# Kernel tuning notes

Hardware: AMD Instinct MI355X
Metric: run time of the kernel (lower is better)

The kernel has to match this reference:

```python
import jax, jax.numpy as jnp
import numpy as np

B, G, GS = 1024, 2000, 25   # batch, num gene groups, group size
H1, H2, C = 1024, 512, 10
EPS = 1e-5


def _xavier(key, shape, fan_in, fan_out):
    lim = np.sqrt(6.0 / (fan_in + fan_out))
    return jax.random.uniform(key, shape, jnp.float32, -lim, lim)


def setup_inputs() -> dict:
    key = jax.random.key(0)
    ks = jax.random.split(key, 8)
    x = jax.random.normal(ks[0], (B, G * GS), jnp.float32)
    # per-group Linear(GS, 1) weights stacked -> block-diagonal grouped GEMM
    gene_w = _xavier(ks[1], (G, GS), GS, 1)
    gene_b = jnp.zeros((G,), jnp.float32)
    W1 = _xavier(ks[2], (G, H1), G, H1)
    b1 = jnp.zeros((H1,), jnp.float32)
    W2 = _xavier(ks[3], (H1, H2), H1, H2)
    b2 = jnp.zeros((H2,), jnp.float32)
    Wout = _xavier(ks[4], (H2, C), H2, C)
    bout = jnp.zeros((C,), jnp.float32)
    Wres = _xavier(ks[5], (G, C), G, C)
    bres = jnp.zeros((C,), jnp.float32)
    gamma1 = jnp.ones((H1,), jnp.float32); beta1 = jnp.zeros((H1,), jnp.float32)
    gamma2 = jnp.ones((H2,), jnp.float32); beta2 = jnp.zeros((H2,), jnp.float32)
    return dict(x=x, gene_w=gene_w, gene_b=gene_b, W1=W1, b1=b1,
                gamma1=gamma1, beta1=beta1, W2=W2, b2=b2,
                gamma2=gamma2, beta2=beta2, Wout=Wout, bout=bout,
                Wres=Wres, bres=bres)


def _batch_norm(h, gamma, beta):
    # training-mode BatchNorm1d: biased batch statistics over axis 0
    mu = jnp.mean(h, axis=0)
    var = jnp.mean(jnp.square(h - mu), axis=0)
    return gamma * (h - mu) * jax.lax.rsqrt(var + EPS) + beta


def reference(x, gene_w, gene_b, W1, b1, gamma1, beta1, W2, b2,
              gamma2, beta2, Wout, bout, Wres, bres):
    # fused replacement for the per-group Linear(GS,1)+ReLU loop + cat
    xg = x.reshape(B, G, GS)
    g = jax.nn.relu(jnp.einsum('bgk,gk->bg', xg, gene_w) + gene_b)  # [B, G]
    h1 = jax.nn.relu(_batch_norm(g @ W1 + b1, gamma1, beta1))       # [B, H1]
    h2 = jax.nn.relu(_batch_norm(h1 @ W2 + b2, gamma2, beta2))      # [B, H2]
    x_main = h2 @ Wout + bout                                       # [B, C]
    x_res = g @ Wres + bres                                         # [B, C]
    return jax.nn.softmax(x_main + x_res, axis=1)
```

## Files before the change

### kernel.cpp

```cpp
#include <hip/hip_runtime.h>
#include <math.h>

#define NB   1024
#define NG   2000
#define NGS  25
#define KP   2048
#define NH1  1024
#define NH2  512
#define NC   10
#define EPSV 1e-5f
#define GPB  200

typedef __attribute__((ext_vector_type(8))) __bf16 bf16x8;
typedef __attribute__((ext_vector_type(4))) float f32x4;
typedef __attribute__((ext_vector_type(8))) unsigned short u16x8;
typedef __attribute__((ext_vector_type(4))) unsigned short u16x4;

__device__ __forceinline__ unsigned short f2bf(float f) {
  union { float f; unsigned u; } v; v.f = f;
  return (unsigned short)((v.u + 0x7fffu + ((v.u >> 16) & 1u)) >> 16);
}
__device__ __forceinline__ float bf2f(unsigned short b) {
  union { unsigned u; float f; } v; v.u = ((unsigned)b) << 16;
  return v.f;
}

__global__ __launch_bounds__(256) void gene_kernel(
    const float* __restrict__ x, const float* __restrict__ gw,
    const float* __restrict__ gb, unsigned short* __restrict__ g_bf) {
  __shared__ float xs[GPB * NGS];
  int b = blockIdx.x;
  int blk = blockIdx.y;
  const float4* src = (const float4*)(x + (size_t)b * (NG * NGS) + blk * (GPB * NGS));
  float4* dst = (float4*)xs;
  for (int i = threadIdx.x; i < (GPB * NGS) / 4; i += 256) dst[i] = src[i];
  __syncthreads();
  int j = threadIdx.x;
  if (j < GPB) {
    int gi = blk * GPB + j;
    const float* wp = gw + gi * NGS;
    const float* xp = xs + j * NGS;
    float acc = 0.f;
#pragma unroll
    for (int k = 0; k < NGS; ++k) acc = fmaf(xp[k], wp[k], acc);
    acc += gb[gi];
    g_bf[(size_t)b * KP + gi] = f2bf(fmaxf(acc, 0.f));
  } else if (blk == (NG / GPB - 1) && j < GPB + (KP - NG)) {
    g_bf[(size_t)b * KP + NG + (j - GPB)] = 0;
  }
}

__global__ __launch_bounds__(256) void convT_dual(
    const float* __restrict__ W1, unsigned short* __restrict__ W1bT,
    const float* __restrict__ W2, unsigned short* __restrict__ W2bT) {
  const float* src; unsigned short* dst; int K, N, Kpad;
  if (blockIdx.z == 0) { src = W1; dst = W1bT; K = NG; N = NH1; Kpad = KP; }
  else {
    src = W2; dst = W2bT; K = NH1; N = NH2; Kpad = NH1;
    if (blockIdx.x >= NH1 / 64 || blockIdx.y >= NH2 / 64) return;
  }
  __shared__ unsigned short ts[64][72];
  int k0 = blockIdx.x * 64, n0 = blockIdx.y * 64;
  int t = threadIdx.x;
  int c4 = (t & 15) * 4;
  int r  = t >> 4;
  for (int rr = r; rr < 64; rr += 16) {
    int k = k0 + rr;
    float4 v = make_float4(0.f, 0.f, 0.f, 0.f);
    if (k < K) v = *(const float4*)&src[(size_t)k * N + n0 + c4];
    ts[rr][c4 + 0] = f2bf(v.x); ts[rr][c4 + 1] = f2bf(v.y);
    ts[rr][c4 + 2] = f2bf(v.z); ts[rr][c4 + 3] = f2bf(v.w);
  }
  __syncthreads();
  int rr8 = (t & 7) * 8;
  int cc  = t >> 3;
  for (int c = cc; c < 64; c += 32) {
    u16x8 val;
#pragma unroll
    for (int i = 0; i < 8; ++i) val[i] = ts[rr8 + i][c];
    *(u16x8*)&dst[(size_t)(n0 + c) * Kpad + k0 + rr8] = val;
  }
}

__global__ __launch_bounds__(256) void gemm1_kernel(
    const unsigned short* __restrict__ A,
    const unsigned short* __restrict__ Bt,
    float* __restrict__ C, float* __restrict__ sum, float* __restrict__ sq,
    int M, int N, int Kp) {
  __shared__ unsigned short As[64][72];
  __shared__ unsigned short Bs[64][72];
  int t = threadIdx.x;
  int m0 = blockIdx.y * 64, n0 = blockIdx.x * 64;
  int wave = t >> 6, lane = t & 63;
  int wm = (wave >> 1) * 32, wn = (wave & 1) * 32;
  int fm = lane & 15, fk = (lane >> 4) * 8;
  int srow = t >> 3, skc = (t & 7) * 8;

  f32x4 acc[2][2];
#pragma unroll
  for (int i = 0; i < 2; ++i)
#pragma unroll
    for (int j = 0; j < 2; ++j) acc[i][j] = (f32x4){0.f, 0.f, 0.f, 0.f};

  const unsigned short* Ap = A + (size_t)(m0 + srow) * Kp + skc;
  const unsigned short* Bp = Bt + (size_t)(n0 + srow) * Kp + skc;
  size_t rstep = 32 * (size_t)Kp;

  u16x8 pa0 = *(const u16x8*)(Ap);
  u16x8 pa1 = *(const u16x8*)(Ap + rstep);
  u16x8 pb0 = *(const u16x8*)(Bp);
  u16x8 pb1 = *(const u16x8*)(Bp + rstep);

  for (int k0 = 0; k0 < Kp; k0 += 64) {
    *(u16x8*)&As[srow][skc]      = pa0;
    *(u16x8*)&As[srow + 32][skc] = pa1;
    *(u16x8*)&Bs[srow][skc]      = pb0;
    *(u16x8*)&Bs[srow + 32][skc] = pb1;
    __syncthreads();
    if (k0 + 64 < Kp) {
      pa0 = *(const u16x8*)(Ap + k0 + 64);
      pa1 = *(const u16x8*)(Ap + k0 + 64 + rstep);
      pb0 = *(const u16x8*)(Bp + k0 + 64);
      pb1 = *(const u16x8*)(Bp + k0 + 64 + rstep);
    }
#pragma unroll
    for (int s = 0; s < 2; ++s) {
      bf16x8 af[2], bfr[2];
      af[0]  = *(const bf16x8*)&As[wm + fm][s * 32 + fk];
      af[1]  = *(const bf16x8*)&As[wm + 16 + fm][s * 32 + fk];
      bfr[0] = *(const bf16x8*)&Bs[wn + fm][s * 32 + fk];
      bfr[1] = *(const bf16x8*)&Bs[wn + 16 + fm][s * 32 + fk];
#pragma unroll
      for (int i = 0; i < 2; ++i)
#pragma unroll
        for (int j = 0; j < 2; ++j)
          acc[i][j] = __builtin_amdgcn_mfma_f32_16x16x32_bf16(
              af[i], bfr[j], acc[i][j], 0, 0, 0);
    }
    __syncthreads();
  }

  int crow = (lane >> 4) * 4, ccol = lane & 15;
#pragma unroll
  for (int j = 0; j < 2; ++j) {
    float s = 0.f, ss = 0.f;
#pragma unroll
    for (int i = 0; i < 2; ++i)
#pragma unroll
      for (int r = 0; r < 4; ++r) {
        float v = acc[i][j][r];
        int m = m0 + wm + i * 16 + crow + r;
        int n = n0 + wn + j * 16 + ccol;
        C[(size_t)m * N + n] = v;
        s += v;
        ss = fmaf(v, v, ss);
      }
    s  += __shfl_down(s, 32, 64);  s  += __shfl_down(s, 16, 64);
    ss += __shfl_down(ss, 32, 64); ss += __shfl_down(ss, 16, 64);
    if (lane < 16) {
      atomicAdd(&sum[n0 + wn + j * 16 + lane], s);
      atomicAdd(&sq[n0 + wn + j * 16 + lane], ss);
    }
  }
}

__global__ __launch_bounds__(256) void gemm2_kernel(
    const float* __restrict__ A,
    const unsigned short* __restrict__ Bt,
    float* __restrict__ C, const float* __restrict__ sum1,
    const float* __restrict__ sq1, const float* __restrict__ gam1,
    const float* __restrict__ bet1, float* __restrict__ sum2,
    float* __restrict__ sq2, int M, int N, int Kp) {
  __shared__ unsigned short As[64][72];
  __shared__ unsigned short Bs[64][72];
  int t = threadIdx.x;
  int m0 = blockIdx.y * 64, n0 = blockIdx.x * 64;
  int wave = t >> 6, lane = t & 63;
  int wm = (wave >> 1) * 32, wn = (wave & 1) * 32;
  int fm = lane & 15, fk = (lane >> 4) * 8;
  int srow = t >> 3, skc = (t & 7) * 8;

  f32x4 acc[2][2];
#pragma unroll
  for (int i = 0; i < 2; ++i)
#pragma unroll
    for (int j = 0; j < 2; ++j) acc[i][j] = (f32x4){0.f, 0.f, 0.f, 0.f};

  const float* Ap = A + (size_t)(m0 + srow) * Kp + skc;
  const unsigned short* Bp = Bt + (size_t)(n0 + srow) * Kp + skc;
  size_t rstepA = 32 * (size_t)Kp;
  size_t rstepB = 32 * (size_t)Kp;

  f32x4 pa[4];
  pa[0] = *(const f32x4*)(Ap);
  pa[1] = *(const f32x4*)(Ap + 4);
  pa[2] = *(const f32x4*)(Ap + rstepA);
  pa[3] = *(const f32x4*)(Ap + rstepA + 4);
  u16x8 pb0 = *(const u16x8*)(Bp);
  u16x8 pb1 = *(const u16x8*)(Bp + rstepB);

  for (int k0 = 0; k0 < Kp; k0 += 64) {
    float sc[8], sh[8];
#pragma unroll
    for (int i = 0; i < 8; ++i) {
      int k = k0 + skc + i;
      float mu  = sum1[k] * (1.f / NB);
      float var = sq1[k] * (1.f / NB) - mu * mu;
      float rs  = rsqrtf(var + EPSV);
      sc[i] = gam1[k] * rs;
      sh[i] = fmaf(-mu, sc[i], bet1[k]);
    }
    u16x8 a0, a1;
#pragma unroll
    for (int i = 0; i < 4; ++i) {
      a0[i]     = f2bf(fmaxf(fmaf(pa[0][i], sc[i],     sh[i]),     0.f));
      a0[i + 4] = f2bf(fmaxf(fmaf(pa[1][i], sc[i + 4], sh[i + 4]), 0.f));
      a1[i]     = f2bf(fmaxf(fmaf(pa[2][i], sc[i],     sh[i]),     0.f));
      a1[i + 4] = f2bf(fmaxf(fmaf(pa[3][i], sc[i + 4], sh[i + 4]), 0.f));
    }
    *(u16x8*)&As[srow][skc]      = a0;
    *(u16x8*)&As[srow + 32][skc] = a1;
    *(u16x8*)&Bs[srow][skc]      = pb0;
    *(u16x8*)&Bs[srow + 32][skc] = pb1;
    __syncthreads();
    if (k0 + 64 < Kp) {
      pa[0] = *(const f32x4*)(Ap + k0 + 64);
      pa[1] = *(const f32x4*)(Ap + k0 + 64 + 4);
      pa[2] = *(const f32x4*)(Ap + k0 + 64 + rstepA);
      pa[3] = *(const f32x4*)(Ap + k0 + 64 + rstepA + 4);
      pb0 = *(const u16x8*)(Bp + k0 + 64);
      pb1 = *(const u16x8*)(Bp + k0 + 64 + rstepB);
    }
#pragma unroll
    for (int s = 0; s < 2; ++s) {
      bf16x8 af[2], bfr[2];
      af[0]  = *(const bf16x8*)&As[wm + fm][s * 32 + fk];
      af[1]  = *(const bf16x8*)&As[wm + 16 + fm][s * 32 + fk];
      bfr[0] = *(const bf16x8*)&Bs[wn + fm][s * 32 + fk];
      bfr[1] = *(const bf16x8*)&Bs[wn + 16 + fm][s * 32 + fk];
#pragma unroll
      for (int i = 0; i < 2; ++i)
#pragma unroll
        for (int j = 0; j < 2; ++j)
          acc[i][j] = __builtin_amdgcn_mfma_f32_16x16x32_bf16(
              af[i], bfr[j], acc[i][j], 0, 0, 0);
    }
    __syncthreads();
  }

  int crow = (lane >> 4) * 4, ccol = lane & 15;
#pragma unroll
  for (int j = 0; j < 2; ++j) {
    float s = 0.f, ss = 0.f;
#pragma unroll
    for (int i = 0; i < 2; ++i)
#pragma unroll
      for (int r = 0; r < 4; ++r) {
        float v = acc[i][j][r];
        int m = m0 + wm + i * 16 + crow + r;
        int n = n0 + wn + j * 16 + ccol;
        C[(size_t)m * N + n] = v;
        s += v;
        ss = fmaf(v, v, ss);
      }
    s  += __shfl_down(s, 32, 64);  s  += __shfl_down(s, 16, 64);
    ss += __shfl_down(ss, 32, 64); ss += __shfl_down(ss, 16, 64);
    if (lane < 16) {
      atomicAdd(&sum2[n0 + wn + j * 16 + lane], s);
      atomicAdd(&sq2[n0 + wn + j * 16 + lane], ss);
    }
  }
}

__global__ __launch_bounds__(256) void final_kernel(
    const float* __restrict__ t2, const float* __restrict__ sum2,
    const float* __restrict__ sq2, const float* __restrict__ gam2,
    const float* __restrict__ bet2, const unsigned short* __restrict__ g_bf,
    const float* __restrict__ Wout, const float* __restrict__ bout,
    const float* __restrict__ Wres, const float* __restrict__ bres,
    float* __restrict__ out) {
  int b = blockIdx.x;
  int t = threadIdx.x;
  float acc[NC] = {};

  if (t < NH2 / 4) {
    float4 tv = *(const float4*)&t2[(size_t)b * NH2 + t * 4];
    float raw[4] = {tv.x, tv.y, tv.z, tv.w};
    float hr[4];
#pragma unroll
    for (int i = 0; i < 4; ++i) {
      int c = t * 4 + i;
      float mu  = sum2[c] * (1.f / NB);
      float var = sq2[c] * (1.f / NB) - mu * mu;
      float rs  = rsqrtf(var + EPSV);
      float scv = gam2[c] * rs;
      hr[i] = fmaxf(fmaf(raw[i], scv, fmaf(-mu, scv, bet2[c])), 0.f);
    }
    const float4* wp = (const float4*)&Wout[t * 4 * NC];
    float w[40];
#pragma unroll
    for (int q = 0; q < 10; ++q) {
      float4 wv = wp[q];
      w[q * 4] = wv.x; w[q * 4 + 1] = wv.y; w[q * 4 + 2] = wv.z; w[q * 4 + 3] = wv.w;
    }
#pragma unroll
    for (int r = 0; r < 4; ++r)
#pragma unroll
      for (int c = 0; c < NC; ++c) acc[c] = fmaf(hr[r], w[r * NC + c], acc[c]);
  }

  for (int u = t; u < NG / 4; u += 256) {
    u16x4 gv = *(const u16x4*)&g_bf[(size_t)b * KP + u * 4];
    float gr[4] = {bf2f(gv[0]), bf2f(gv[1]), bf2f(gv[2]), bf2f(gv[3])};
    const float4* wp = (const float4*)&Wres[u * 4 * NC];
    float w[40];
#pragma unroll
    for (int q = 0; q < 10; ++q) {
      float4 wv = wp[q];
      w[q * 4] = wv.x; w[q * 4 + 1] = wv.y; w[q * 4 + 2] = wv.z; w[q * 4 + 3] = wv.w;
    }
#pragma unroll
    for (int r = 0; r < 4; ++r)
#pragma unroll
      for (int c = 0; c < NC; ++c) acc[c] = fmaf(gr[r], w[r * NC + c], acc[c]);
  }

  __shared__ float red[4][NC];
  __shared__ float logits[NC];
  int lane = t & 63, wave = t >> 6;
#pragma unroll
  for (int c = 0; c < NC; ++c) {
    float v = acc[c];
    for (int off = 32; off > 0; off >>= 1) v += __shfl_down(v, off, 64);
    if (lane == 0) red[wave][c] = v;
  }
  __syncthreads();
  if (t < NC)
    logits[t] = red[0][t] + red[1][t] + red[2][t] + red[3][t] + bout[t] + bres[t];
  __syncthreads();
  if (t == 0) {
    float mx = logits[0];
#pragma unroll
    for (int c = 1; c < NC; ++c) mx = fmaxf(mx, logits[c]);
    float e[NC], s = 0.f;
#pragma unroll
    for (int c = 0; c < NC; ++c) { e[c] = expf(logits[c] - mx); s += e[c]; }
    float inv = 1.f / s;
#pragma unroll
    for (int c = 0; c < NC; ++c) out[(size_t)b * NC + c] = e[c] * inv;
  }
}

extern "C" void kernel_launch(void* const* d_in, const int* in_sizes, int n_in,
                              void* d_out, int out_size, void* d_ws, size_t ws_size,
                              hipStream_t stream) {
  const float* x      = (const float*)d_in[0];
  const float* gw     = (const float*)d_in[1];
  const float* gb     = (const float*)d_in[2];
  const float* W1     = (const float*)d_in[3];
  const float* gamma1 = (const float*)d_in[5];
  const float* beta1  = (const float*)d_in[6];
  const float* W2     = (const float*)d_in[7];
  const float* gamma2 = (const float*)d_in[9];
  const float* beta2  = (const float*)d_in[10];
  const float* Wout   = (const float*)d_in[11];
  const float* bout   = (const float*)d_in[12];
  const float* Wres   = (const float*)d_in[13];
  const float* bres   = (const float*)d_in[14];
  float* out = (float*)d_out;

  char* p = (char*)d_ws;
  unsigned short* g_bf = (unsigned short*)p; p += (size_t)NB * KP * 2;
  unsigned short* W1bT = (unsigned short*)p; p += (size_t)NH1 * KP * 2;
  unsigned short* W2bT = (unsigned short*)p; p += (size_t)NH2 * NH1 * 2;
  float* t1 = (float*)p; p += (size_t)NB * NH1 * 4;
  float* t2 = (float*)p; p += (size_t)NB * NH2 * 4;
  float* stats = (float*)p;
  float* sum1 = stats, *sq1 = stats + 1024, *sum2 = stats + 2048, *sq2 = stats + 2560;

  hipMemsetAsync(stats, 0, 3072 * sizeof(float), stream);

  convT_dual<<<dim3(KP / 64, NH1 / 64, 2), 256, 0, stream>>>(W1, W1bT, W2, W2bT);

  gene_kernel<<<dim3(NB, NG / GPB), 256, 0, stream>>>(x, gw, gb, g_bf);

  gemm1_kernel<<<dim3(NH1 / 64, NB / 64), 256, 0, stream>>>(
      g_bf, W1bT, t1, sum1, sq1, NB, NH1, KP);

  gemm2_kernel<<<dim3(NH2 / 64, NB / 64), 256, 0, stream>>>(
      t1, W2bT, t2, sum1, sq1, gamma1, beta1, sum2, sq2, NB, NH2, NH1);

  final_kernel<<<NB, 256, 0, stream>>>(t2, sum2, sq2, gamma2, beta2, g_bf,
                                       Wout, bout, Wres, bres, out);
}
```

Measured before the change: 372.5 us.

## Merge prep kernels into one launch and shrink GEMM tiles for more blocks

Merges the gene reduction, the weight transpose/bf16 conversion and the stats zeroing into one prep kernel launched over an 11-row grid, removing a memset and a kernel launch. GEMM1 tiles shrink from 64x64 to 32x64 and GEMM2 tiles from 64x64 to 32x32, so each GEMM launches more blocks to fill the CUs. The cost is less operand reuse per block, more redundant global loads, and more atomic stat updates.

```diff
diff --git a/kernel.cpp b/kernel.cpp
--- a/kernel.cpp
+++ b/kernel.cpp
@@ -25,43 +25,52 @@
   return v.f;
 }
 
-__global__ __launch_bounds__(256) void gene_kernel(
+__global__ __launch_bounds__(256) void prep_kernel(
     const float* __restrict__ x, const float* __restrict__ gw,
-    const float* __restrict__ gb, unsigned short* __restrict__ g_bf) {
-  __shared__ float xs[GPB * NGS];
-  int b = blockIdx.x;
-  int blk = blockIdx.y;
-  const float4* src = (const float4*)(x + (size_t)b * (NG * NGS) + blk * (GPB * NGS));
-  float4* dst = (float4*)xs;
-  for (int i = threadIdx.x; i < (GPB * NGS) / 4; i += 256) dst[i] = src[i];
-  __syncthreads();
-  int j = threadIdx.x;
-  if (j < GPB) {
-    int gi = blk * GPB + j;
-    const float* wp = gw + gi * NGS;
-    const float* xp = xs + j * NGS;
-    float acc = 0.f;
-#pragma unroll
-    for (int k = 0; k < NGS; ++k) acc = fmaf(xp[k], wp[k], acc);
-    acc += gb[gi];
-    g_bf[(size_t)b * KP + gi] = f2bf(fmaxf(acc, 0.f));
-  } else if (blk == (NG / GPB - 1) && j < GPB + (KP - NG)) {
-    g_bf[(size_t)b * KP + NG + (j - GPB)] = 0;
-  }
-}
-
-__global__ __launch_bounds__(256) void convT_dual(
+    const float* __restrict__ gb, unsigned short* __restrict__ g_bf,
     const float* __restrict__ W1, unsigned short* __restrict__ W1bT,
-    const float* __restrict__ W2, unsigned short* __restrict__ W2bT) {
-  const float* src; unsigned short* dst; int K, N, Kpad;
-  if (blockIdx.z == 0) { src = W1; dst = W1bT; K = NG; N = NH1; Kpad = KP; }
-  else {
-    src = W2; dst = W2bT; K = NH1; N = NH2; Kpad = NH1;
-    if (blockIdx.x >= NH1 / 64 || blockIdx.y >= NH2 / 64) return;
-  }
-  __shared__ unsigned short ts[64][72];
-  int k0 = blockIdx.x * 64, n0 = blockIdx.y * 64;
+    const float* __restrict__ W2, unsigned short* __restrict__ W2bT,
+    float* __restrict__ stats) {
+  __shared__ char smem[GPB * NGS * 4];
   int t = threadIdx.x;
+
+  if (blockIdx.y < 10) {
+    float* xs = (float*)smem;
+    int b = blockIdx.x;
+    int blk = blockIdx.y;
+    const float4* src = (const float4*)(x + (size_t)b * (NG * NGS) + blk * (GPB * NGS));
+    float4* dst = (float4*)xs;
+    for (int i = t; i < (GPB * NGS) / 4; i += 256) dst[i] = src[i];
+    __syncthreads();
+    if (t < GPB) {
+      int gi = blk * GPB + t;
+      const float* wp = gw + gi * NGS;
+      const float* xp = xs + t * NGS;
+      float acc = 0.f;
+#pragma unroll
+      for (int k = 0; k < NGS; ++k) acc = fmaf(xp[k], wp[k], acc);
+      acc += gb[gi];
+      g_bf[(size_t)b * KP + gi] = f2bf(fmaxf(acc, 0.f));
+    } else if (blk == 9 && t < GPB + (KP - NG)) {
+      g_bf[(size_t)b * KP + NG + (t - GPB)] = 0;
+    }
+    return;
+  }
+
+  int bx = blockIdx.x;
+  if (bx == 640) {
+    for (int i = t; i < 3072; i += 256) stats[i] = 0.f;
+    return;
+  }
+  const float* src; unsigned short* dst; int K, N, Kpad, k0, n0;
+  if (bx < 512)      { src = W1; dst = W1bT; K = NG;  N = NH1; Kpad = KP;
+                       k0 = (bx & 31) * 64; n0 = (bx >> 5) * 64; }
+  else if (bx < 640) { int xi = bx - 512;
+                       src = W2; dst = W2bT; K = NH1; N = NH2; Kpad = NH1;
+                       k0 = (xi & 15) * 64; n0 = (xi >> 4) * 64; }
+  else return;
+
+  unsigned short (*ts)[72] = (unsigned short (*)[72])smem;
   int c4 = (t & 15) * 4;
   int r  = t >> 4;
   for (int rr = r; rr < 64; rr += 16) {
@@ -87,55 +96,44 @@
     const unsigned short* __restrict__ Bt,
     float* __restrict__ C, float* __restrict__ sum, float* __restrict__ sq,
     int M, int N, int Kp) {
-  __shared__ unsigned short As[64][72];
+  __shared__ unsigned short As[32][72];
   __shared__ unsigned short Bs[64][72];
   int t = threadIdx.x;
-  int m0 = blockIdx.y * 64, n0 = blockIdx.x * 64;
+  int m0 = blockIdx.y * 32, n0 = blockIdx.x * 64;
   int wave = t >> 6, lane = t & 63;
-  int wm = (wave >> 1) * 32, wn = (wave & 1) * 32;
+  int wm = (wave >> 1) * 16, wn = (wave & 1) * 32;
   int fm = lane & 15, fk = (lane >> 4) * 8;
   int srow = t >> 3, skc = (t & 7) * 8;
 
-  f32x4 acc[2][2];
-#pragma unroll
-  for (int i = 0; i < 2; ++i)
-#pragma unroll
-    for (int j = 0; j < 2; ++j) acc[i][j] = (f32x4){0.f, 0.f, 0.f, 0.f};
+  f32x4 acc[2];
+  acc[0] = (f32x4){0.f, 0.f, 0.f, 0.f};
+  acc[1] = (f32x4){0.f, 0.f, 0.f, 0.f};
 
   const unsigned short* Ap = A + (size_t)(m0 + srow) * Kp + skc;
   const unsigned short* Bp = Bt + (size_t)(n0 + srow) * Kp + skc;
   size_t rstep = 32 * (size_t)Kp;
 
   u16x8 pa0 = *(const u16x8*)(Ap);
-  u16x8 pa1 = *(const u16x8*)(Ap + rstep);
   u16x8 pb0 = *(const u16x8*)(Bp);
   u16x8 pb1 = *(const u16x8*)(Bp + rstep);
 
   for (int k0 = 0; k0 < Kp; k0 += 64) {
     *(u16x8*)&As[srow][skc]      = pa0;
-    *(u16x8*)&As[srow + 32][skc] = pa1;
     *(u16x8*)&Bs[srow][skc]      = pb0;
     *(u16x8*)&Bs[srow + 32][skc] = pb1;
     __syncthreads();
     if (k0 + 64 < Kp) {
       pa0 = *(const u16x8*)(Ap + k0 + 64);
-      pa1 = *(const u16x8*)(Ap + k0 + 64 + rstep);
       pb0 = *(const u16x8*)(Bp + k0 + 64);
       pb1 = *(const u16x8*)(Bp + k0 + 64 + rstep);
     }
 #pragma unroll
     for (int s = 0; s < 2; ++s) {
-      bf16x8 af[2], bfr[2];
-      af[0]  = *(const bf16x8*)&As[wm + fm][s * 32 + fk];
-      af[1]  = *(const bf16x8*)&As[wm + 16 + fm][s * 32 + fk];
-      bfr[0] = *(const bf16x8*)&Bs[wn + fm][s * 32 + fk];
-      bfr[1] = *(const bf16x8*)&Bs[wn + 16 + fm][s * 32 + fk];
-#pragma unroll
-      for (int i = 0; i < 2; ++i)
-#pragma unroll
-        for (int j = 0; j < 2; ++j)
-          acc[i][j] = __builtin_amdgcn_mfma_f32_16x16x32_bf16(
-              af[i], bfr[j], acc[i][j], 0, 0, 0);
+      bf16x8 af = *(const bf16x8*)&As[wm + fm][s * 32 + fk];
+      bf16x8 b0 = *(const bf16x8*)&Bs[wn + fm][s * 32 + fk];
+      bf16x8 b1 = *(const bf16x8*)&Bs[wn + 16 + fm][s * 32 + fk];
+      acc[0] = __builtin_amdgcn_mfma_f32_16x16x32_bf16(af, b0, acc[0], 0, 0, 0);
+      acc[1] = __builtin_amdgcn_mfma_f32_16x16x32_bf16(af, b1, acc[1], 0, 0, 0);
     }
     __syncthreads();
   }
@@ -145,16 +143,14 @@
   for (int j = 0; j < 2; ++j) {
     float s = 0.f, ss = 0.f;
 #pragma unroll
-    for (int i = 0; i < 2; ++i)
-#pragma unroll
-      for (int r = 0; r < 4; ++r) {
-        float v = acc[i][j][r];
-        int m = m0 + wm + i * 16 + crow + r;
-        int n = n0 + wn + j * 16 + ccol;
-        C[(size_t)m * N + n] = v;
-        s += v;
-        ss = fmaf(v, v, ss);
-      }
+    for (int r = 0; r < 4; ++r) {
+      float v = acc[j][r];
+      int m = m0 + wm + crow + r;
+      int n = n0 + wn + j * 16 + ccol;
+      C[(size_t)m * N + n] = v;
+      s += v;
+      ss = fmaf(v, v, ss);
+    }
     s  += __shfl_down(s, 32, 64);  s  += __shfl_down(s, 16, 64);
     ss += __shfl_down(ss, 32, 64); ss += __shfl_down(ss, 16, 64);
     if (lane < 16) {
@@ -171,33 +167,23 @@
     const float* __restrict__ sq1, const float* __restrict__ gam1,
     const float* __restrict__ bet1, float* __restrict__ sum2,
     float* __restrict__ sq2, int M, int N, int Kp) {
-  __shared__ unsigned short As[64][72];
-  __shared__ unsigned short Bs[64][72];
+  __shared__ unsigned short As[32][72];
+  __shared__ unsigned short Bs[32][72];
   int t = threadIdx.x;
-  int m0 = blockIdx.y * 64, n0 = blockIdx.x * 64;
+  int m0 = blockIdx.y * 32, n0 = blockIdx.x * 32;
   int wave = t >> 6, lane = t & 63;
-  int wm = (wave >> 1) * 32, wn = (wave & 1) * 32;
+  int wm = (wave >> 1) * 16, wn = (wave & 1) * 16;
   int fm = lane & 15, fk = (lane >> 4) * 8;
   int srow = t >> 3, skc = (t & 7) * 8;
 
-  f32x4 acc[2][2];
-#pragma unroll
-  for (int i = 0; i < 2; ++i)
-#pragma unroll
-    for (int j = 0; j < 2; ++j) acc[i][j] = (f32x4){0.f, 0.f, 0.f, 0.f};
+  f32x4 acc = (f32x4){0.f, 0.f, 0.f, 0.f};
 
   const float* Ap = A + (size_t)(m0 + srow) * Kp + skc;
   const unsigned short* Bp = Bt + (size_t)(n0 + srow) * Kp + skc;
-  size_t rstepA = 32 * (size_t)Kp;
-  size_t rstepB = 32 * (size_t)Kp;
-
-  f32x4 pa[4];
-  pa[0] = *(const f32x4*)(Ap);
-  pa[1] = *(const f32x4*)(Ap + 4);
-  pa[2] = *(const f32x4*)(Ap + rstepA);
-  pa[3] = *(const f32x4*)(Ap + rstepA + 4);
+
+  f32x4 pa0 = *(const f32x4*)(Ap);
+  f32x4 pa1 = *(const f32x4*)(Ap + 4);
   u16x8 pb0 = *(const u16x8*)(Bp);
-  u16x8 pb1 = *(const u16x8*)(Bp + rstepB);
 
   for (int k0 = 0; k0 < Kp; k0 += 64) {
     float sc[8], sh[8];
@@ -210,65 +196,45 @@
       sc[i] = gam1[k] * rs;
       sh[i] = fmaf(-mu, sc[i], bet1[k]);
     }
-    u16x8 a0, a1;
+    u16x8 a0;
 #pragma unroll
     for (int i = 0; i < 4; ++i) {
-      a0[i]     = f2bf(fmaxf(fmaf(pa[0][i], sc[i],     sh[i]),     0.f));
-      a0[i + 4] = f2bf(fmaxf(fmaf(pa[1][i], sc[i + 4], sh[i + 4]), 0.f));
-      a1[i]     = f2bf(fmaxf(fmaf(pa[2][i], sc[i],     sh[i]),     0.f));
-      a1[i + 4] = f2bf(fmaxf(fmaf(pa[3][i], sc[i + 4], sh[i + 4]), 0.f));
-    }
-    *(u16x8*)&As[srow][skc]      = a0;
-    *(u16x8*)&As[srow + 32][skc] = a1;
-    *(u16x8*)&Bs[srow][skc]      = pb0;
-    *(u16x8*)&Bs[srow + 32][skc] = pb1;
+      a0[i]     = f2bf(fmaxf(fmaf(pa0[i], sc[i],     sh[i]),     0.f));
+      a0[i + 4] = f2bf(fmaxf(fmaf(pa1[i], sc[i + 4], sh[i + 4]), 0.f));
+    }
+    *(u16x8*)&As[srow][skc] = a0;
+    *(u16x8*)&Bs[srow][skc] = pb0;
     __syncthreads();
     if (k0 + 64 < Kp) {
-      pa[0] = *(const f32x4*)(Ap + k0 + 64);
-      pa[1] = *(const f32x4*)(Ap + k0 + 64 + 4);
-      pa[2] = *(const f32x4*)(Ap + k0 + 64 + rstepA);
-      pa[3] = *(const f32x4*)(Ap + k0 + 64 + rstepA + 4);
+      pa0 = *(const f32x4*)(Ap + k0 + 64);
+      pa1 = *(const f32x4*)(Ap + k0 + 64 + 4);
       pb0 = *(const u16x8*)(Bp + k0 + 64);
-      pb1 = *(const u16x8*)(Bp + k0 + 64 + rstepB);
     }
 #pragma unroll
     for (int s = 0; s < 2; ++s) {
-      bf16x8 af[2], bfr[2];
-      af[0]  = *(const bf16x8*)&As[wm + fm][s * 32 + fk];
-      af[1]  = *(const bf16x8*)&As[wm + 16 + fm][s * 32 + fk];
-      bfr[0] = *(const bf16x8*)&Bs[wn + fm][s * 32 + fk];
-      bfr[1] = *(const bf16x8*)&Bs[wn + 16 + fm][s * 32 + fk];
-#pragma unroll
-      for (int i = 0; i < 2; ++i)
-#pragma unroll
-        for (int j = 0; j < 2; ++j)
-          acc[i][j] = __builtin_amdgcn_mfma_f32_16x16x32_bf16(
-              af[i], bfr[j], acc[i][j], 0, 0, 0);
+      bf16x8 af = *(const bf16x8*)&As[wm + fm][s * 32 + fk];
+      bf16x8 bf = *(const bf16x8*)&Bs[wn + fm][s * 32 + fk];
+      acc = __builtin_amdgcn_mfma_f32_16x16x32_bf16(af, bf, acc, 0, 0, 0);
     }
     __syncthreads();
   }
 
   int crow = (lane >> 4) * 4, ccol = lane & 15;
-#pragma unroll
-  for (int j = 0; j < 2; ++j) {
-    float s = 0.f, ss = 0.f;
-#pragma unroll
-    for (int i = 0; i < 2; ++i)
-#pragma unroll
-      for (int r = 0; r < 4; ++r) {
-        float v = acc[i][j][r];
-        int m = m0 + wm + i * 16 + crow + r;
-        int n = n0 + wn + j * 16 + ccol;
-        C[(size_t)m * N + n] = v;
-        s += v;
-        ss = fmaf(v, v, ss);
-      }
-    s  += __shfl_down(s, 32, 64);  s  += __shfl_down(s, 16, 64);
-    ss += __shfl_down(ss, 32, 64); ss += __shfl_down(ss, 16, 64);
-    if (lane < 16) {
-      atomicAdd(&sum2[n0 + wn + j * 16 + lane], s);
-      atomicAdd(&sq2[n0 + wn + j * 16 + lane], ss);
-    }
+  float s = 0.f, ss = 0.f;
+#pragma unroll
+  for (int r = 0; r < 4; ++r) {
+    float v = acc[r];
+    int m = m0 + wm + crow + r;
+    int n = n0 + wn + ccol;
+    C[(size_t)m * N + n] = v;
+    s += v;
+    ss = fmaf(v, v, ss);
+  }
+  s  += __shfl_down(s, 32, 64);  s  += __shfl_down(s, 16, 64);
+  ss += __shfl_down(ss, 32, 64); ss += __shfl_down(ss, 16, 64);
+  if (lane < 16) {
+    atomicAdd(&sum2[n0 + wn + lane], s);
+    atomicAdd(&sq2[n0 + wn + lane], ss);
   }
 }
 
@@ -378,16 +344,13 @@
   float* stats = (float*)p;
   float* sum1 = stats, *sq1 = stats + 1024, *sum2 = stats + 2048, *sq2 = stats + 2560;
 
-  hipMemsetAsync(stats, 0, 3072 * sizeof(float), stream);
-
-  convT_dual<<<dim3(KP / 64, NH1 / 64, 2), 256, 0, stream>>>(W1, W1bT, W2, W2bT);
-
-  gene_kernel<<<dim3(NB, NG / GPB), 256, 0, stream>>>(x, gw, gb, g_bf);
-
-  gemm1_kernel<<<dim3(NH1 / 64, NB / 64), 256, 0, stream>>>(
+  prep_kernel<<<dim3(NB, 11), 256, 0, stream>>>(x, gw, gb, g_bf,
+                                                W1, W1bT, W2, W2bT, stats);
+
+  gemm1_kernel<<<dim3(NH1 / 64, NB / 32), 256, 0, stream>>>(
       g_bf, W1bT, t1, sum1, sq1, NB, NH1, KP);
 
-  gemm2_kernel<<<dim3(NH2 / 64, NB / 64), 256, 0, stream>>>(
+  gemm2_kernel<<<dim3(NH2 / 32, NB / 32), 256, 0, stream>>>(
       t1, W2bT, t2, sum1, sq1, gamma1, beta1, sum2, sq2, NB, NH2, NH1);
 
   final_kernel<<<NB, 256, 0, stream>>>(t2, sum2, sq2, gamma2, beta2, g_bf,
```

Result: no change. 366.2 us (-1.7%).
